# Performance work log

Measured on AMD Instinct MI355X. Metric: run time of the kernel, lower is better.

Reference implementation:

```python
import jax, jax.numpy as jnp
import numpy as np

NUM_GROUPS = 32
NUM_HEADS = 8  # channels=512 / num_head_channels=64
EPS = 1e-5


def group_norm(x, gamma, beta):
    # x: [B, C, T]
    b, c, t = x.shape
    xg = x.reshape(b, NUM_GROUPS, (c // NUM_GROUPS) * t)
    mean = xg.mean(axis=-1, keepdims=True)
    var = xg.var(axis=-1, keepdims=True)
    xg = (xg - mean) * jax.lax.rsqrt(var + EPS)
    return xg.reshape(b, c, t) * gamma[None, :, None] + beta[None, :, None]


def setup_inputs() -> dict:
    key = jax.random.key(0)
    ks = jax.random.split(key, 8)
    B, C, H, W = 16, 512, 32, 32
    E = 1024
    x = jax.random.normal(ks[0], (B, C, H, W), dtype=jnp.float32)
    emb = jax.random.normal(ks[1], (B, E), dtype=jnp.float32)
    gn_gamma = jnp.ones((C,), jnp.float32)
    gn_beta = jnp.zeros((C,), jnp.float32)
    # FiLM: Linear(emb_channels, 2*channels), weight init std=0.001, bias zero
    emb_w = jax.random.normal(ks[2], (2 * C, E), dtype=jnp.float32) * 0.001
    emb_b = jnp.zeros((2 * C,), jnp.float32)
    # conv1x1 qkv: [3C, C]
    qkv_w = jax.random.normal(ks[3], (3 * C, C), dtype=jnp.float32) * (1.0 / np.sqrt(C))
    qkv_b = jnp.zeros((3 * C,), jnp.float32)
    # proj_out conv1x1 (zero-init in original; use small random so grads flow)
    proj_w = jax.random.normal(ks[4], (C, C), dtype=jnp.float32) * 0.02
    proj_b = jnp.zeros((C,), jnp.float32)
    return dict(x=x, emb=emb, gn_gamma=gn_gamma, gn_beta=gn_beta,
                emb_w=emb_w, emb_b=emb_b, qkv_w=qkv_w, qkv_b=qkv_b,
                proj_w=proj_w, proj_b=proj_b)


def reference(x, emb, gn_gamma, gn_beta, emb_w, emb_b, qkv_w, qkv_b, proj_w, proj_b):
    b, c, h_sp, w_sp = x.shape
    t = h_sp * w_sp
    xr = x.reshape(b, c, t)
    h = group_norm(xr, gn_gamma, gn_beta)
    # FiLM conditioning
    e = jax.nn.silu(emb) @ emb_w.T + emb_b  # [B, 2C]
    scale, shift = jnp.split(e, 2, axis=1)
    h = h * (1.0 + scale[:, :, None]) + shift[:, :, None]
    # conv1x1 QKV
    qkv = jnp.einsum('oc,bct->bot', qkv_w, h) + qkv_b[None, :, None]  # [B, 3C, T]
    ch = c // NUM_HEADS
    qkv = qkv.reshape(b * NUM_HEADS, 3 * ch, t)  # legacy head ordering
    q, k, v = jnp.split(qkv, 3, axis=1)
    s = 1.0 / jnp.sqrt(jnp.sqrt(jnp.float32(ch)))
    w = jnp.einsum('bct,bcs->bts', q * s, k * s)  # [B*H, T, T]
    w = jax.nn.softmax(w, axis=-1)
    a = jnp.einsum('bts,bcs->bct', w, v).reshape(b, c, t)
    out = jnp.einsum('oc,bct->bot', proj_w, a) + proj_b[None, :, None]
    return (xr + out).reshape(b, c, h_sp, w_sp)
```

## Files before the change

### kernel.cpp

```cpp
#include <hip/hip_runtime.h>
#include <hip/hip_bf16.h>

typedef __hip_bfloat16 bf16;
typedef __attribute__((ext_vector_type(8))) short short8;
typedef __attribute__((ext_vector_type(4))) float f32x4;
typedef __attribute__((ext_vector_type(4))) unsigned short us4;
typedef __attribute__((ext_vector_type(2))) unsigned short us2;

#define B_  16
#define C_  512
#define T_  1024
#define G_  32
#define CPG 16
#define E_  1024
#define NH  8
#define CH  64
#define CT  (C_ * T_)

__device__ __forceinline__ float b2f(bf16 v) { return __bfloat162float(v); }
__device__ __forceinline__ bf16  f2b(float v) { return __float2bfloat16(v); }
__device__ __forceinline__ unsigned short fbits(float v) {
  bf16 t = f2b(v);
  return *reinterpret_cast<unsigned short*>(&t);
}
__device__ __forceinline__ unsigned short fbits_fast(float v) {
  unsigned int u = __builtin_bit_cast(unsigned int, v);
  u += 0x7fff + ((u >> 16) & 1);
  return (unsigned short)(u >> 16);
}
__device__ __forceinline__ bf16 f2b_fast(float v) {
  unsigned short s = fbits_fast(v);
  return *reinterpret_cast<bf16*>(&s);
}

__device__ __forceinline__ void gload16(const void* g, void* l) {
  __builtin_amdgcn_global_load_lds(
      (const __attribute__((address_space(1))) void*)g,
      (__attribute__((address_space(3))) void*)l, 16, 0, 0);
}

__global__ __launch_bounds__(256) void convert_w_kernel(
    const float* __restrict__ qkv_w, const float* __restrict__ proj_w,
    bf16* __restrict__ wq, bf16* __restrict__ wp) {
  int i4 = blockIdx.x * 256 + threadIdx.x;
  const int NQ4 = (3 * C_ * C_) / 4;
  const float* src;
  unsigned short* dst;
  int off;
  if (i4 < NQ4) {
    src = qkv_w; dst = (unsigned short*)wq; off = i4;
  } else {
    src = proj_w; dst = (unsigned short*)wp; off = i4 - NQ4;
  }
  float4 v = *(const float4*)(src + (size_t)off * 4);
  us4 pk = {fbits_fast(v.x), fbits_fast(v.y), fbits_fast(v.z),
            fbits_fast(v.w)};
  *(us4*)(dst + (size_t)off * 4) = pk;
}

__global__ __launch_bounds__(256) void film2_kernel(
    const float* __restrict__ emb, const float* __restrict__ emb_w,
    const float* __restrict__ emb_b, float* __restrict__ e_out) {
  __shared__ float S[B_ * E_];
  int tid = threadIdx.x;
  float4* S4 = (float4*)S;
  const float4* e4 = (const float4*)emb;
  for (int i = tid; i < (B_ * E_) / 4; i += 256) {
    float4 v = e4[i];
    float4 o;
    o.x = v.x / (1.f + __expf(-v.x));
    o.y = v.y / (1.f + __expf(-v.y));
    o.z = v.z / (1.f + __expf(-v.z));
    o.w = v.w / (1.f + __expf(-v.w));
    S4[i] = o;
  }
  __syncthreads();
  int wave = tid >> 6, lane = tid & 63;
  int j = blockIdx.x * 4 + wave;
  const float4* w4p = (const float4*)(emb_w + (size_t)j * E_);
  float4 w4[4];
#pragma unroll
  for (int k = 0; k < 4; k++) w4[k] = w4p[k * 64 + lane];
  float bias = emb_b[j];
  for (int b = 0; b < B_; b++) {
    const float4* Sb = (const float4*)(S + b * E_);
    float acc = 0.f;
#pragma unroll
    for (int k = 0; k < 4; k++) {
      float4 s = Sb[k * 64 + lane];
      acc += w4[k].x * s.x + w4[k].y * s.y + w4[k].z * s.z + w4[k].w * s.w;
    }
#pragma unroll
    for (int off = 1; off < 64; off <<= 1) acc += __shfl_xor(acc, off, 64);
    if (lane == 0) e_out[b * (2 * C_) + j] = acc + bias;
  }
}

__global__ __launch_bounds__(256) void gn_stats_kernel(
    const float* __restrict__ x, float* __restrict__ mean_buf,
    float* __restrict__ rstd_buf) {
  int bg = blockIdx.x;
  const float4* b4 = (const float4*)(x + (size_t)bg * (CPG * T_));
  int tid = threadIdx.x;
  float s = 0.f, sq = 0.f;
  for (int i = tid; i < (CPG * T_) / 4; i += 256) {
    float4 v = b4[i];
    s += v.x + v.y + v.z + v.w;
    sq += v.x * v.x + v.y * v.y + v.z * v.z + v.w * v.w;
  }
  for (int off = 32; off > 0; off >>= 1) {
    s += __shfl_down(s, off, 64);
    sq += __shfl_down(sq, off, 64);
  }
  __shared__ float ss[4], ssq[4];
  int wid = tid >> 6, lane = tid & 63;
  if (lane == 0) { ss[wid] = s; ssq[wid] = sq; }
  __syncthreads();
  if (tid == 0) {
    float S = ss[0] + ss[1] + ss[2] + ss[3];
    float Q = ssq[0] + ssq[1] + ssq[2] + ssq[3];
    const float inv_n = 1.f / (CPG * T_);
    float m = S * inv_n;
    float var = Q * inv_n - m * m;
    mean_buf[bg] = m;
    rstd_buf[bg] = rsqrtf(fmaxf(var, 0.f) + 1e-5f);
  }
}

__global__ __launch_bounds__(256) void norm_film_t2(
    const float* __restrict__ x, const float* __restrict__ mean_buf,
    const float* __restrict__ rstd_buf, const float* __restrict__ gamma,
    const float* __restrict__ beta, const float* __restrict__ e_buf,
    bf16* __restrict__ h, int b0) {
  __shared__ unsigned short S[64][66];
  __shared__ float pm[64], pr[64], pa[64];
  int t0 = blockIdx.x * 64;
  int c0 = blockIdx.y * 64;
  int bl = blockIdx.z;
  int b = b0 + bl;
  int tid = threadIdx.x;
  if (tid < 64) {
    int c = c0 + tid;
    int g = c >> 4;
    float m = mean_buf[b * G_ + g];
    float r = rstd_buf[b * G_ + g];
    float sc = 1.f + e_buf[b * 2 * C_ + c];
    float sh = e_buf[b * 2 * C_ + C_ + c];
    pm[tid] = m;
    pr[tid] = r * gamma[c] * sc;
    pa[tid] = beta[c] * sc + sh;
  }
  __syncthreads();
  const float* xb = x + ((size_t)b * C_ + c0) * T_ + t0;
#pragma unroll
  for (int p = 0; p < 4; p++) {
    int i = p * 256 + tid;
    int cl = i >> 4, t4 = (i & 15) * 4;
    float4 v = *(const float4*)(xb + (size_t)cl * T_ + t4);
    float m = pm[cl], r = pr[cl], ad = pa[cl];
    us2 lo = {fbits_fast((v.x - m) * r + ad), fbits_fast((v.y - m) * r + ad)};
    us2 hi = {fbits_fast((v.z - m) * r + ad), fbits_fast((v.w - m) * r + ad)};
    *(us2*)&S[cl][t4] = lo;
    *(us2*)&S[cl][t4 + 2] = hi;
  }
  __syncthreads();
  unsigned short* hg = (unsigned short*)h + ((size_t)bl * T_ + t0) * C_ + c0;
#pragma unroll
  for (int p = 0; p < 2; p++) {
    int i = p * 256 + tid;
    int tr = i >> 3, c8 = (i & 7) * 8;
    unsigned int w0 = (unsigned int)S[c8 + 0][tr] |
                      ((unsigned int)S[c8 + 1][tr] << 16);
    unsigned int w1 = (unsigned int)S[c8 + 2][tr] |
                      ((unsigned int)S[c8 + 3][tr] << 16);
    unsigned int w2 = (unsigned int)S[c8 + 4][tr] |
                      ((unsigned int)S[c8 + 5][tr] << 16);
    unsigned int w3 = (unsigned int)S[c8 + 6][tr] |
                      ((unsigned int)S[c8 + 7][tr] << 16);
    int4 pk = {(int)w0, (int)w1, (int)w2, (int)w3};
    *(int4*)(hg + (size_t)tr * C_ + c8) = pk;
  }
}

#define ST_STRIDE 264
__global__ __launch_bounds__(256) void qkv_gemm_mfma3(
    const bf16* __restrict__ h, const bf16* __restrict__ wq,
    const float* __restrict__ qkv_b, bf16* __restrict__ qb,
    bf16* __restrict__ kb, bf16* __restrict__ vb) {
  __shared__ __align__(16) unsigned short LB[20480];
  int bl = blockIdx.z;
  int tst = blockIdx.y;
  int o0 = blockIdx.x * 64;
  int tb = tst * 256;
  int tid = threadIdx.x;
  int wave = tid >> 6, lane = tid & 63;
  int col = lane & 15, quad = lane >> 4;
  int cs = col & 7;
  int w64 = wave * 64;
  const unsigned short* hg = (const unsigned short*)h + (size_t)bl * T_ * C_;
  const unsigned short* wg = (const unsigned short*)wq;
  char* lds = (char*)LB;
  f32x4 acc[4][4];
  for (int i = 0; i < 4; i++)
    for (int j = 0; j < 4; j++) acc[i][j] = f32x4{0, 0, 0, 0};
  for (int c0 = 0; c0 < C_; c0 += 64) {
    __syncthreads();
#pragma unroll
    for (int p = 0; p < 8; p++) {
      int i = p * 256 + tid;
      int row = i >> 3;
      int sci = (i & 7) ^ (row & 7);
      gload16(hg + (size_t)(tb + row) * C_ + c0 + sci * 8,
              lds + (p * 256 + wave * 64) * 16);
    }
#pragma unroll
    for (int p = 0; p < 2; p++) {
      int i = p * 256 + tid;
      int row = i >> 3;
      int sci = (i & 7) ^ (row & 7);
      gload16(wg + (size_t)(o0 + row) * C_ + c0 + sci * 8,
              lds + 32768 + (p * 256 + wave * 64) * 16);
    }
    __syncthreads();
#pragma unroll
    for (int ks = 0; ks < 2; ks++) {
      short8 af[4], bfr[4];
#pragma unroll
      for (int mt = 0; mt < 4; mt++)
        af[mt] = *(const short8*)&LB[(w64 + mt * 16 + col) * 64 +
                                     (((ks * 4 + quad) ^ cs) << 3)];
#pragma unroll
      for (int nt = 0; nt < 4; nt++)
        bfr[nt] = *(const short8*)&LB[16384 + (nt * 16 + col) * 64 +
                                      (((ks * 4 + quad) ^ cs) << 3)];
#pragma unroll
      for (int mt = 0; mt < 4; mt++)
#pragma unroll
        for (int nt = 0; nt < 4; nt++)
          acc[mt][nt] = __builtin_amdgcn_mfma_f32_16x16x32_bf16(
              af[mt], bfr[nt], acc[mt][nt], 0, 0, 0);
    }
  }
  int sec = (o0 >> 6) % 3;
  int hd = o0 / 192;
  const float s = 0.35355339059327373f;
  const float sq = s * 1.4426950408889634f;
  if (sec < 2) {
    bf16* dst = (sec == 0) ? qb : kb;
    float sc = (sec == 0) ? sq : s;
    size_t hb = (size_t)(bl * NH + hd) * T_ * CH;
    for (int mt = 0; mt < 4; mt++) {
      for (int r = 0; r < 4; r++) {
        int t = tb + w64 + mt * 16 + quad * 4 + r;
        for (int nt = 0; nt < 4; nt++) {
          int ch = nt * 16 + col;
          dst[hb + (size_t)t * CH + ch] =
              f2b_fast((acc[mt][nt][r] + qkv_b[o0 + ch]) * sc);
        }
      }
    }
  } else {
    __syncthreads();
    for (int mt = 0; mt < 4; mt++) {
      for (int r = 0; r < 4; r++) {
        int tl = w64 + mt * 16 + quad * 4 + r;
        for (int nt = 0; nt < 4; nt++) {
          int ch = nt * 16 + col;
          LB[ch * ST_STRIDE + tl] =
              fbits_fast(acc[mt][nt][r] + qkv_b[o0 + ch]);
        }
      }
    }
    __syncthreads();
    int rr = tid >> 2, csx = (tid & 3) * 64;
    size_t base = ((size_t)(bl * NH + hd) * CH + rr) * T_ + tb + csx;
    unsigned short* vg = (unsigned short*)vb;
    for (int j = 0; j < 8; j++)
      *(int4*)(vg + base + j * 8) = *(const int4*)&LB[rr * ST_STRIDE + csx + j * 8];
  }
}

__global__ __launch_bounds__(256, 4) void attn_mfma7(
    const bf16* __restrict__ qb, const bf16* __restrict__ kb,
    const bf16* __restrict__ vb, bf16* __restrict__ a, int nbh) {
  __shared__ __align__(16) unsigned short LB[20480];
  int bid = blockIdx.x;
  int bh = bid % nbh;
  int qt0 = (bid / nbh) * 128;
  int tid = threadIdx.x;
  int wave = tid >> 6, lane = tid & 63;
  int col = lane & 15, quad = lane >> 4;
  int cs = col & 7;
  int ps = (col >> 1) & 3;
  const unsigned short* qg = (const unsigned short*)qb;
  const unsigned short* kg = (const unsigned short*)kb;
  const unsigned short* vg = (const unsigned short*)vb;
  const size_t tmaj = (size_t)bh * T_ * CH;
  const size_t cmaj = (size_t)bh * CH * T_;
  char* lds = (char*)LB;

  int qrow = qt0 + wave * 16 + col;
  short8 bq0[2], bq1[2];
#pragma unroll
  for (int u = 0; u < 2; u++) {
    const unsigned short* qp = qg + tmaj + (size_t)(qrow + u * 64) * CH;
    bq0[u] = *(const short8*)(qp + quad * 8);
    bq1[u] = *(const short8*)(qp + 32 + quad * 8);
  }
  f32x4 Ot0[4], Ot1[4];
#pragma unroll
  for (int mt = 0; mt < 4; mt++) {
    Ot0[mt] = f32x4{0, 0, 0, 0};
    Ot1[mt] = f32x4{0, 0, 0, 0};
  }
  const short ob = (short)0x3F80;
  short8 ones = {ob, ob, ob, ob, ob, ob, ob, ob};
  f32x4 La0 = f32x4{0, 0, 0, 0}, La1 = f32x4{0, 0, 0, 0};
  unsigned short* pw0 = LB + 16384 + wave * 512 + col * 32;
  unsigned short* pw1 = pw0 + 2048;

#define STAGE(buf, tt)                                                        \
  do {                                                                        \
    int s0_ = (tt) * 64;                                                      \
    const unsigned short* kt_ = kg + tmaj + (size_t)s0_ * CH;                 \
    const unsigned short* vt_ = vg + cmaj + s0_;                              \
    _Pragma("unroll") for (int cc = 0; cc < 2; cc++) {                        \
      int i_ = cc * 256 + tid;                                                \
      int row_ = i_ >> 3;                                                     \
      int sci_ = (i_ & 7) ^ (row_ & 7);                                       \
      int wb_ = (cc * 256 + wave * 64) * 16;       \
      gload16(kt_ + (size_t)row_ * CH + sci_ * 8, lds + (buf) * 8192 + wb_);  \
      gload16(vt_ + (size_t)row_ * T_ + sci_ * 8,                             \
              lds + 16384 + (buf) * 8192 + wb_);                              \
    }                                                                         \
  } while (0)

  STAGE(0, 0);
  __syncthreads();
  int cur = 0;
  for (int t = 0; t < 16; t++) {
    if (t < 15) STAGE(cur ^ 1, t + 1);
    const char* ksb = lds + cur * 8192;
    const char* vtb = lds + 16384 + cur * 8192;
    f32x4 St0[4], St1[4];
#pragma unroll
    for (int mt = 0; mt < 4; mt++) {
      St0[mt] = f32x4{0, 0, 0, 0};
      St1[mt] = f32x4{0, 0, 0, 0};
    }
    __builtin_amdgcn_s_setprio(1);
#pragma unroll
    for (int mt = 0; mt < 4; mt++) {
      int rb = (mt * 16 + col) * 128;
      short8 ak0 = *(const short8*)(ksb + rb + ((quad ^ cs) << 4));
      short8 ak1 = *(const short8*)(ksb + rb + (((quad + 4) ^ cs) << 4));
      St0[mt] = __builtin_amdgcn_mfma_f32_16x16x32_bf16(ak0, bq0[0], St0[mt], 0, 0, 0);
      St1[mt] = __builtin_amdgcn_mfma_f32_16x16x32_bf16(ak0, bq0[1], St1[mt], 0, 0, 0);
      St0[mt] = __builtin_amdgcn_mfma_f32_16x16x32_bf16(ak1, bq1[0], St0[mt], 0, 0, 0);
      St1[mt] = __builtin_amdgcn_mfma_f32_16x16x32_bf16(ak1, bq1[1], St1[mt], 0, 0, 0);
    }
    __builtin_amdgcn_s_setprio(0);
#pragma unroll
    for (int mt = 0; mt < 4; mt++)
#pragma unroll
      for (int r = 0; r < 4; r++) {
        St0[mt][r] = __builtin_amdgcn_exp2f(St0[mt][r]);
        St1[mt][r] = __builtin_amdgcn_exp2f(St1[mt][r]);
      }
#pragma unroll
    for (int kc = 0; kc < 2; kc++) {
#pragma unroll
      for (int mh = 0; mh < 2; mh++) {
        int mt = kc * 2 + mh;
        int wsw = (((2 * mh + (quad >> 1)) ^ ps) << 3) + (quad & 1) * 4;
        uint2 k0 = {(unsigned int)fbits_fast(St0[mt][0]) |
                        ((unsigned int)fbits_fast(St0[mt][1]) << 16),
                    (unsigned int)fbits_fast(St0[mt][2]) |
                        ((unsigned int)fbits_fast(St0[mt][3]) << 16)};
      uint2 k1 = {(unsigned int)fbits_fast(St1[mt][0]) |
                        ((unsigned int)fbits_fast(St1[mt][1]) << 16),
                    (unsigned int)fbits_fast(St1[mt][2]) |
                        ((unsigned int)fbits_fast(St1[mt][3]) << 16)};
        *(uint2*)(pw0 + wsw) = k0;
        *(uint2*)(pw1 + wsw) = k1;
      }
      int rsw = (quad ^ ps) << 3;
      short8 bp0 = *(const short8*)(pw0 + rsw);
      short8 bp1 = *(const short8*)(pw1 + rsw);
      __builtin_amdgcn_s_setprio(1);
      La0 = __builtin_amdgcn_mfma_f32_16x16x32_bf16(ones, bp0, La0, 0, 0, 0);
      La1 = __builtin_amdgcn_mfma_f32_16x16x32_bf16(ones, bp1, La1, 0, 0, 0);
#pragma unroll
      for (int mt = 0; mt < 4; mt++) {
        short8 av = *(const short8*)(vtb + (mt * 16 + col) * 128 +
                                     (((kc * 4 + quad) ^ cs) << 4));
        Ot0[mt] = __builtin_amdgcn_mfma_f32_16x16x32_bf16(av, bp0, Ot0[mt], 0, 0, 0);
        Ot1[mt] = __builtin_amdgcn_mfma_f32_16x16x32_bf16(av, bp1, Ot1[mt], 0, 0, 0);
      }
      __builtin_amdgcn_s_setprio(0);
    }
    __syncthreads();
    cur ^= 1;
  }
#undef STAGE
  int bl = bh >> 3, hd = bh & 7;
  unsigned short* ag = (unsigned short*)a;
#pragma unroll
  for (int u = 0; u < 2; u++) {
    float inv = 1.f / ((u == 0) ? La0[0] : La1[0]);
    const f32x4* Ou = (u == 0) ? Ot0 : Ot1;
    size_t rowb = ((size_t)bl * T_ + qrow + u * 64) * C_ + hd * CH;
#pragma unroll
    for (int mt = 0; mt < 4; mt++) {
      unsigned int d0 = (unsigned int)fbits_fast(Ou[mt][0] * inv) |
                        ((unsigned int)fbits_fast(Ou[mt][1] * inv) << 16);
      unsigned int d1 = (unsigned int)fbits_fast(Ou[mt][2] * inv) |
                        ((unsigned int)fbits_fast(Ou[mt][3] * inv) << 16);
      uint2 pk = {d0, d1};
      *(uint2*)(ag + rowb + mt * 16 + quad * 4) = pk;
    }
  }
}

__global__ __launch_bounds__(256) void proj_mfma3(
    const bf16* __restrict__ a, const bf16* __restrict__ wp,
    const float* __restrict__ proj_b, const float* __restrict__ x,
    float* __restrict__ out, int b0) {
  __shared__ __align__(16) unsigned short LB[8192];
  int bl = blockIdx.z;
  int b = b0 + bl;
  int o0 = blockIdx.y * 64;
  int t0 = blockIdx.x * 64;
  int tid = threadIdx.x;
  int wave = tid >> 6, lane = tid & 63;
  int col = lane & 15, quad = lane >> 4;
  int cs = col & 7;
  int m0 = wave * 16;
  const unsigned short* ag = (const unsigned short*)a + (size_t)bl * T_ * C_;
  const unsigned short* wg = (const unsigned short*)wp;
  char* lds = (char*)LB;
  f32x4 acc[4] = {f32x4{0,0,0,0}, f32x4{0,0,0,0}, f32x4{0,0,0,0}, f32x4{0,0,0,0}};
  for (int c0 = 0; c0 < C_; c0 += 64) {
    __syncthreads();
#pragma unroll
    for (int cc = 0; cc < 2; cc++) {
      int i = cc * 256 + tid;
      int row = i >> 3;
      int sci = (i & 7) ^ (row & 7);
      int wb = (cc * 256 + wave * 64) * 16;
      gload16(ag + (size_t)(t0 + row) * C_ + c0 + sci * 8, lds + wb);
      gload16(wg + (size_t)(o0 + row) * C_ + c0 + sci * 8, lds + 8192 + wb);
    }
    __syncthreads();
#pragma unroll
    for (int ks = 0; ks < 2; ks++) {
      short8 aw = *(const short8*)&LB[4096 + (m0 + col) * 64 +
                                      (((ks * 4 + quad) ^ cs) << 3)];
#pragma unroll
      for (int nt = 0; nt < 4; nt++) {
        short8 ba = *(const short8*)&LB[(nt * 16 + col) * 64 +
                                        (((ks * 4 + quad) ^ cs) << 3)];
        acc[nt] = __builtin_amdgcn_mfma_f32_16x16x32_bf16(aw, ba, acc[nt], 0, 0, 0);
      }
    }
  }
  for (int r = 0; r < 4; r++) {
    int o = o0 + m0 + quad * 4 + r;
    float bias = proj_b[o];
    size_t rowb = ((size_t)b * C_ + o) * T_ + t0;
    for (int nt = 0; nt < 4; nt++) {
      int t = nt * 16 + col;
      out[rowb + t] = x[rowb + t] + acc[nt][r] + bias;
    }
  }
}

extern "C" void kernel_launch(void* const* d_in, const int* in_sizes, int n_in,
                              void* d_out, int out_size, void* d_ws,
                              size_t ws_size, hipStream_t stream) {
  const float* x      = (const float*)d_in[0];
  const float* emb    = (const float*)d_in[1];
  const float* gamma  = (const float*)d_in[2];
  const float* beta   = (const float*)d_in[3];
  const float* emb_w  = (const float*)d_in[4];
  const float* emb_b  = (const float*)d_in[5];
  const float* qkv_w  = (const float*)d_in[6];
  const float* qkv_b  = (const float*)d_in[7];
  const float* proj_w = (const float*)d_in[8];
  const float* proj_b = (const float*)d_in[9];
  float* out = (float*)d_out;

  float* e_buf    = (float*)d_ws;
  float* mean_buf = e_buf + B_ * 2 * C_;
  float* rstd_buf = mean_buf + B_ * G_;
  bf16*  wq_bf    = (bf16*)((char*)d_ws + 131072);
  bf16*  wp_bf    = wq_bf + (size_t)3 * C_ * C_;
  const size_t FIXED_BYTES = 131072 + (size_t)4 * C_ * C_ * sizeof(bf16);
  bf16* pool = (bf16*)((char*)d_ws + FIXED_BYTES);

  size_t avail = ws_size > FIXED_BYTES ? ws_size - FIXED_BYTES : 0;
  int NB = 16;
  while (NB > 1 && (size_t)4 * NB * CT * sizeof(bf16) > avail) NB >>= 1;

  bf16* h_buf = pool;
  bf16* q_buf = h_buf + (size_t)NB * CT;
  bf16* k_buf = q_buf + (size_t)NB * CT;
  bf16* v_buf = k_buf + (size_t)NB * CT;

  convert_w_kernel<<<dim3(1024), 256, 0, stream>>>(qkv_w, proj_w, wq_bf, wp_bf);
  film2_kernel<<<dim3(256), 256, 0, stream>>>(emb, emb_w, emb_b, e_buf);
  gn_stats_kernel<<<dim3(B_ * G_), 256, 0, stream>>>(x, mean_buf, rstd_buf);
  for (int b0 = 0; b0 < B_; b0 += NB) {
    norm_film_t2<<<dim3(16, 8, NB), 256, 0, stream>>>(
        x, mean_buf, rstd_buf, gamma, beta, e_buf, h_buf, b0);
    qkv_gemm_mfma3<<<dim3(24, 4, NB), 256, 0, stream>>>(h_buf, wq_bf, qkv_b,
                                                        q_buf, k_buf, v_buf);
    int nbh = NB * NH;
    attn_mfma7<<<dim3(8 * nbh), 256, 0, stream>>>(q_buf, k_buf, v_buf, h_buf,
                                                  nbh);
    proj_mfma3<<<dim3(16, 8, NB), 256, 0, stream>>>(h_buf, wp_bf, proj_b, x,
                                                    out, b0);
  }
}
```

Before: 240.6 us.

## Use packed bf16 convert, wider GN stats blocks, and full-batch workspace path

Replaces the manual round-to-nearest bf16 packing with the hardware v_cvt_pk_bf16_f32 instruction in the weight conversion, norm, attention P-store and output paths. The GroupNorm statistics kernel now uses 1024-thread blocks with a fixed unrolled load loop. The host adds a path that processes all 16 batches in one pass when the workspace is large enough. If the scratch area does not fit, that path borrows the output buffer and a freed q buffer to hold intermediates. This is meant to cut conversion ALU work and per-chunk launch overhead, at the cost of aliasing complexity.

```diff
diff --git a/kernel.cpp b/kernel.cpp
--- a/kernel.cpp
+++ b/kernel.cpp
@@ -18,11 +18,6 @@
 #define CT  (C_ * T_)
 
 __device__ __forceinline__ float b2f(bf16 v) { return __bfloat162float(v); }
-__device__ __forceinline__ bf16  f2b(float v) { return __float2bfloat16(v); }
-__device__ __forceinline__ unsigned short fbits(float v) {
-  bf16 t = f2b(v);
-  return *reinterpret_cast<unsigned short*>(&t);
-}
 __device__ __forceinline__ unsigned short fbits_fast(float v) {
   unsigned int u = __builtin_bit_cast(unsigned int, v);
   u += 0x7fff + ((u >> 16) & 1);
@@ -31,6 +26,11 @@
 __device__ __forceinline__ bf16 f2b_fast(float v) {
   unsigned short s = fbits_fast(v);
   return *reinterpret_cast<bf16*>(&s);
+}
+__device__ __forceinline__ unsigned int cvtpk(float lo, float hi) {
+  unsigned int r;
+  asm("v_cvt_pk_bf16_f32 %0, %1, %2" : "=v"(r) : "v"(lo), "v"(hi));
+  return r;
 }
 
 __device__ __forceinline__ void gload16(const void* g, void* l) {
@@ -53,9 +53,16 @@
     src = proj_w; dst = (unsigned short*)wp; off = i4 - NQ4;
   }
   float4 v = *(const float4*)(src + (size_t)off * 4);
-  us4 pk = {fbits_fast(v.x), fbits_fast(v.y), fbits_fast(v.z),
-            fbits_fast(v.w)};
-  *(us4*)(dst + (size_t)off * 4) = pk;
+  uint2 pk = {cvtpk(v.x, v.y), cvtpk(v.z, v.w)};
+  *(uint2*)(dst + (size_t)off * 4) = pk;
+}
+
+__global__ __launch_bounds__(256) void convert_one(
+    const float* __restrict__ src, bf16* __restrict__ dst) {
+  int i4 = blockIdx.x * 256 + threadIdx.x;
+  float4 v = *(const float4*)(src + (size_t)i4 * 4);
+  uint2 pk = {cvtpk(v.x, v.y), cvtpk(v.z, v.w)};
+  *(uint2*)((unsigned short*)dst + (size_t)i4 * 4) = pk;
 }
 
 __global__ __launch_bounds__(256) void film2_kernel(
@@ -96,15 +103,16 @@
   }
 }
 
-__global__ __launch_bounds__(256) void gn_stats_kernel(
+__global__ __launch_bounds__(1024) void gn_stats_kernel(
     const float* __restrict__ x, float* __restrict__ mean_buf,
     float* __restrict__ rstd_buf) {
   int bg = blockIdx.x;
   const float4* b4 = (const float4*)(x + (size_t)bg * (CPG * T_));
   int tid = threadIdx.x;
   float s = 0.f, sq = 0.f;
-  for (int i = tid; i < (CPG * T_) / 4; i += 256) {
-    float4 v = b4[i];
+#pragma unroll
+  for (int p = 0; p < 4; p++) {
+    float4 v = b4[p * 1024 + tid];
     s += v.x + v.y + v.z + v.w;
     sq += v.x * v.x + v.y * v.y + v.z * v.z + v.w * v.w;
   }
@@ -112,13 +120,14 @@
     s += __shfl_down(s, off, 64);
     sq += __shfl_down(sq, off, 64);
   }
-  __shared__ float ss[4], ssq[4];
+  __shared__ float ss[16], ssq[16];
   int wid = tid >> 6, lane = tid & 63;
   if (lane == 0) { ss[wid] = s; ssq[wid] = sq; }
   __syncthreads();
   if (tid == 0) {
-    float S = ss[0] + ss[1] + ss[2] + ss[3];
-    float Q = ssq[0] + ssq[1] + ssq[2] + ssq[3];
+    float S = 0.f, Q = 0.f;
+#pragma unroll
+    for (int w = 0; w < 16; w++) { S += ss[w]; Q += ssq[w]; }
     const float inv_n = 1.f / (CPG * T_);
     float m = S * inv_n;
     float var = Q * inv_n - m * m;
@@ -158,10 +167,9 @@
     int cl = i >> 4, t4 = (i & 15) * 4;
     float4 v = *(const float4*)(xb + (size_t)cl * T_ + t4);
     float m = pm[cl], r = pr[cl], ad = pa[cl];
-    us2 lo = {fbits_fast((v.x - m) * r + ad), fbits_fast((v.y - m) * r + ad)};
-    us2 hi = {fbits_fast((v.z - m) * r + ad), fbits_fast((v.w - m) * r + ad)};
-    *(us2*)&S[cl][t4] = lo;
-    *(us2*)&S[cl][t4 + 2] = hi;
+    *(unsigned int*)&S[cl][t4] = cvtpk((v.x - m) * r + ad, (v.y - m) * r + ad);
+    *(unsigned int*)&S[cl][t4 + 2] =
+        cvtpk((v.z - m) * r + ad, (v.w - m) * r + ad);
   }
   __syncthreads();
   unsigned short* hg = (unsigned short*)h + ((size_t)bl * T_ + t0) * C_ + c0;
@@ -280,7 +288,7 @@
   }
 }
 
-__global__ __launch_bounds__(256, 4) void attn_mfma7(
+__global__ __launch_bounds__(256, 4) void attn_mfma8(
     const bf16* __restrict__ qb, const bf16* __restrict__ kb,
     const bf16* __restrict__ vb, bf16* __restrict__ a, int nbh) {
   __shared__ __align__(16) unsigned short LB[20480];
@@ -373,14 +381,10 @@
       for (int mh = 0; mh < 2; mh++) {
         int mt = kc * 2 + mh;
         int wsw = (((2 * mh + (quad >> 1)) ^ ps) << 3) + (quad & 1) * 4;
-        uint2 k0 = {(unsigned int)fbits_fast(St0[mt][0]) |
-                        ((unsigned int)fbits_fast(St0[mt][1]) << 16),
-                    (unsigned int)fbits_fast(St0[mt][2]) |
-                        ((unsigned int)fbits_fast(St0[mt][3]) << 16)};
-      uint2 k1 = {(unsigned int)fbits_fast(St1[mt][0]) |
-                        ((unsigned int)fbits_fast(St1[mt][1]) << 16),
-                    (unsigned int)fbits_fast(St1[mt][2]) |
-                        ((unsigned int)fbits_fast(St1[mt][3]) << 16)};
+        uint2 k0 = {cvtpk(St0[mt][0], St0[mt][1]),
+                    cvtpk(St0[mt][2], St0[mt][3])};
+        uint2 k1 = {cvtpk(St1[mt][0], St1[mt][1]),
+                    cvtpk(St1[mt][2], St1[mt][3])};
         *(uint2*)(pw0 + wsw) = k0;
         *(uint2*)(pw1 + wsw) = k1;
       }
@@ -412,11 +416,8 @@
     size_t rowb = ((size_t)bl * T_ + qrow + u * 64) * C_ + hd * CH;
 #pragma unroll
     for (int mt = 0; mt < 4; mt++) {
-      unsigned int d0 = (unsigned int)fbits_fast(Ou[mt][0] * inv) |
-                        ((unsigned int)fbits_fast(Ou[mt][1] * inv) << 16);
-      unsigned int d1 = (unsigned int)fbits_fast(Ou[mt][2] * inv) |
-                        ((unsigned int)fbits_fast(Ou[mt][3] * inv) << 16);
-      uint2 pk = {d0, d1};
+      uint2 pk = {cvtpk(Ou[mt][0] * inv, Ou[mt][1] * inv),
+                  cvtpk(Ou[mt][2] * inv, Ou[mt][3] * inv)};
       *(uint2*)(ag + rowb + mt * 16 + quad * 4) = pk;
     }
   }
@@ -490,35 +491,72 @@
   const float* proj_b = (const float*)d_in[9];
   float* out = (float*)d_out;
 
-  float* e_buf    = (float*)d_ws;
-  float* mean_buf = e_buf + B_ * 2 * C_;
-  float* rstd_buf = mean_buf + B_ * G_;
-  bf16*  wq_bf    = (bf16*)((char*)d_ws + 131072);
-  bf16*  wp_bf    = wq_bf + (size_t)3 * C_ * C_;
-  const size_t FIXED_BYTES = 131072 + (size_t)4 * C_ * C_ * sizeof(bf16);
-  bf16* pool = (bf16*)((char*)d_ws + FIXED_BYTES);
-
-  size_t avail = ws_size > FIXED_BYTES ? ws_size - FIXED_BYTES : 0;
-  int NB = 16;
-  while (NB > 1 && (size_t)4 * NB * CT * sizeof(bf16) > avail) NB >>= 1;
-
-  bf16* h_buf = pool;
-  bf16* q_buf = h_buf + (size_t)NB * CT;
-  bf16* k_buf = q_buf + (size_t)NB * CT;
-  bf16* v_buf = k_buf + (size_t)NB * CT;
-
-  convert_w_kernel<<<dim3(1024), 256, 0, stream>>>(qkv_w, proj_w, wq_bf, wp_bf);
-  film2_kernel<<<dim3(256), 256, 0, stream>>>(emb, emb_w, emb_b, e_buf);
-  gn_stats_kernel<<<dim3(B_ * G_), 256, 0, stream>>>(x, mean_buf, rstd_buf);
-  for (int b0 = 0; b0 < B_; b0 += NB) {
-    norm_film_t2<<<dim3(16, 8, NB), 256, 0, stream>>>(
-        x, mean_buf, rstd_buf, gamma, beta, e_buf, h_buf, b0);
-    qkv_gemm_mfma3<<<dim3(24, 4, NB), 256, 0, stream>>>(h_buf, wq_bf, qkv_b,
+  const size_t BUF16 = (size_t)16 * CT * sizeof(bf16);
+  const size_t FULL4 = 4 * BUF16;
+  const size_t SCR   = 131072 + (size_t)4 * C_ * C_ * sizeof(bf16);
+
+  if (ws_size >= FULL4) {
+    bf16* h_buf = (bf16*)d_ws;
+    bf16* q_buf = h_buf + BUF16 / sizeof(bf16);
+    bf16* k_buf = q_buf + BUF16 / sizeof(bf16);
+    bf16* v_buf = k_buf + BUF16 / sizeof(bf16);
+    bool inWs = ws_size >= FULL4 + SCR;
+    char* scr = inWs ? ((char*)d_ws + FULL4) : (char*)d_out;
+    float* e_buf    = (float*)scr;
+    float* mean_buf = e_buf + B_ * 2 * C_;
+    float* rstd_buf = mean_buf + B_ * G_;
+    bf16*  wq_bf    = (bf16*)(scr + 131072);
+    bf16*  wp_bf;
+
+    if (inWs) {
+      wp_bf = wq_bf + (size_t)3 * C_ * C_;
+      convert_w_kernel<<<dim3(1024), 256, 0, stream>>>(qkv_w, proj_w, wq_bf,
+                                                       wp_bf);
+    } else {
+      wp_bf = q_buf;
+      convert_one<<<dim3(768), 256, 0, stream>>>(qkv_w, wq_bf);
+    }
+    film2_kernel<<<dim3(256), 256, 0, stream>>>(emb, emb_w, emb_b, e_buf);
+    gn_stats_kernel<<<dim3(B_ * G_), 1024, 0, stream>>>(x, mean_buf, rstd_buf);
+    norm_film_t2<<<dim3(16, 8, 16), 256, 0, stream>>>(
+        x, mean_buf, rstd_buf, gamma, beta, e_buf, h_buf, 0);
+    qkv_gemm_mfma3<<<dim3(24, 4, 16), 256, 0, stream>>>(h_buf, wq_bf, qkv_b,
                                                         q_buf, k_buf, v_buf);
-    int nbh = NB * NH;
-    attn_mfma7<<<dim3(8 * nbh), 256, 0, stream>>>(q_buf, k_buf, v_buf, h_buf,
-                                                  nbh);
-    proj_mfma3<<<dim3(16, 8, NB), 256, 0, stream>>>(h_buf, wp_bf, proj_b, x,
-                                                    out, b0);
-  }
-}
+    attn_mfma8<<<dim3(8 * 128), 256, 0, stream>>>(q_buf, k_buf, v_buf, h_buf,
+                                                  128);
+    if (!inWs)
+      convert_one<<<dim3(256), 256, 0, stream>>>(proj_w, wp_bf);
+    proj_mfma3<<<dim3(16, 8, 16), 256, 0, stream>>>(h_buf, wp_bf, proj_b, x,
+                                                    out, 0);
+  } else {
+    float* e_buf    = (float*)d_ws;
+    float* mean_buf = e_buf + B_ * 2 * C_;
+    float* rstd_buf = mean_buf + B_ * G_;
+    bf16*  wq_bf    = (bf16*)((char*)d_ws + 131072);
+    bf16*  wp_bf    = wq_bf + (size_t)3 * C_ * C_;
+    bf16* pool = (bf16*)((char*)d_ws + SCR);
+    size_t avail = ws_size > SCR ? ws_size - SCR : 0;
+    int NB = 16;
+    while (NB > 1 && (size_t)4 * NB * CT * sizeof(bf16) > avail) NB >>= 1;
+    bf16* h_buf = pool;
+    bf16* q_buf = h_buf + (size_t)NB * CT;
+    bf16* k_buf = q_buf + (size_t)NB * CT;
+    bf16* v_buf = k_buf + (size_t)NB * CT;
+
+    convert_w_kernel<<<dim3(1024), 256, 0, stream>>>(qkv_w, proj_w, wq_bf,
+                                                     wp_bf);
+    film2_kernel<<<dim3(256), 256, 0, stream>>>(emb, emb_w, emb_b, e_buf);
+    gn_stats_kernel<<<dim3(B_ * G_), 1024, 0, stream>>>(x, mean_buf, rstd_buf);
+    for (int b0 = 0; b0 < B_; b0 += NB) {
+      norm_film_t2<<<dim3(16, 8, NB), 256, 0, stream>>>(
+          x, mean_buf, rstd_buf, gamma, beta, e_buf, h_buf, b0);
+      qkv_gemm_mfma3<<<dim3(24, 4, NB), 256, 0, stream>>>(h_buf, wq_bf, qkv_b,
+                                                          q_buf, k_buf, v_buf);
+      int nbh = NB * NH;
+      attn_mfma8<<<dim3(8 * nbh), 256, 0, stream>>>(q_buf, k_buf, v_buf,
+                                                    h_buf, nbh);
+      proj_mfma3<<<dim3(16, 8, NB), 256, 0, stream>>>(h_buf, wp_bf, proj_b, x,
+                                                      out, b0);
+    }
+  }
+}
```

After: 227.9 us. -5.3%, faster.
